# Performance work log

Measured on AMD Instinct MI355X. Metric: run time of the kernel, lower is better.

## Reference

```python
import jax, jax.numpy as jnp
import numpy as np

NEG_SLOPE = 0.2  # PyG GATv2Conv default negative_slope
HEADS = 4


def _gatv2_layer(x, src, dst, Wl, bl, Wr, br, att, bias):
    """GATv2Conv, concat=False (mean over heads), add_self_loops handled by caller.
    x: [N, Fin]; src/dst: [E] (message src -> dst); Wl/Wr: [Fin, H*C]; att: [H, C].
    """
    N = x.shape[0]
    H, C = att.shape
    xl = (x @ Wl + bl).reshape(N, H, C)  # source-side transform
    xr = (x @ Wr + br).reshape(N, H, C)  # target-side transform
    e = jax.nn.leaky_relu(xl[src] + xr[dst], NEG_SLOPE)          # [E, H, C]
    logits = jnp.einsum('ehc,hc->eh', e, att)                     # [E, H]
    # segment softmax over incoming edges of each target node
    m = jax.ops.segment_max(logits, dst, num_segments=N)          # [N, H]
    a = jnp.exp(logits - m[dst])
    denom = jax.ops.segment_sum(a, dst, num_segments=N)
    alpha = a / denom[dst]                                        # [E, H]
    out = jax.ops.segment_sum(alpha[:, :, None] * xl[src], dst, num_segments=N)  # [N, H, C]
    return out.mean(axis=1) + bias                                # concat=False -> head mean


def _glorot(k, shape):
    fan_in, fan_out = shape[0], shape[1] if len(shape) > 1 else shape[0]
    s = jnp.sqrt(2.0 / (fan_in + fan_out)).astype(jnp.float32)
    return jax.random.normal(k, shape, jnp.float32) * s


def setup_inputs() -> dict:
    key = jax.random.key(0)
    ks = jax.random.split(key, 24)
    N, E = 50000, 512000
    x = jax.random.normal(ks[0], (N, 9), jnp.float32)
    src = jax.random.randint(ks[1], (E,), 0, N, dtype=jnp.int32)
    dst = jax.random.randint(ks[2], (E,), 0, N, dtype=jnp.int32)
    dst = jnp.where(src == dst, (dst + 1) % N, dst)  # PyG removes self-loops then re-adds them
    edge_index = jnp.stack([src, dst])
    dims = [(9, 64), (64, 64), (64, 128)]  # (Fin, C_out) per layer
    inp = {'x': x, 'edge_index': edge_index}
    ki = 3
    for i, (fi, co) in enumerate(dims):
        inp[f'Wl{i}'] = _glorot(ks[ki], (fi, HEADS * co)); ki += 1
        inp[f'bl{i}'] = jnp.zeros((HEADS * co,), jnp.float32)
        inp[f'Wr{i}'] = _glorot(ks[ki], (fi, HEADS * co)); ki += 1
        inp[f'br{i}'] = jnp.zeros((HEADS * co,), jnp.float32)
        inp[f'att{i}'] = _glorot(ks[ki], (HEADS, co)); ki += 1
        inp[f'b{i}'] = jnp.zeros((co,), jnp.float32)
    return inp


def reference(x, edge_index, Wl0, bl0, Wr0, br0, att0, b0,
              Wl1, bl1, Wr1, br1, att1, b1,
              Wl2, bl2, Wr2, br2, att2, b2):
    N = x.shape[0]
    loops = jnp.arange(N, dtype=edge_index.dtype)
    src = jnp.concatenate([edge_index[0], loops])  # add self-loops (PyG default)
    dst = jnp.concatenate([edge_index[1], loops])
    h = _gatv2_layer(x, src, dst, Wl0, bl0, Wr0, br0, att0, b0)
    h = jax.nn.relu(h)  # dropout: eval mode -> identity
    h = _gatv2_layer(h, src, dst, Wl1, bl1, Wr1, br1, att1, b1)
    h = jax.nn.relu(h)
    out = _gatv2_layer(h, src, dst, Wl2, bl2, Wr2, br2, att2, b2)
    return out
```

## Files before the change

kernel.cpp:

```cpp
#include <hip/hip_runtime.h>
#include <hip/hip_bf16.h>


typedef __attribute__((ext_vector_type(8))) short bf16x8;
typedef __attribute__((ext_vector_type(4))) float f32x4;

__device__ __forceinline__ float bflo(unsigned w) { return __uint_as_float(w << 16); }
__device__ __forceinline__ float bfhi(unsigned w) { return __uint_as_float(w & 0xffff0000u); }
__device__ __forceinline__ unsigned short f2bf(float v) {
    unsigned u = __float_as_uint(v);
    u = (u + 0x7fff + ((u >> 16) & 1)) >> 16;
    return (unsigned short)u;
}
__device__ __forceinline__ float bf2f(unsigned short h) {
    return __uint_as_float((unsigned)h << 16);
}


__global__ void zero_int_k(int* p, int n) {
    int i = blockIdx.x * 256 + threadIdx.x;
    if (i < n) p[i] = 0;
}

__global__ void count_k(const int* __restrict__ dst, int* __restrict__ cnt,
                        int E, int EP) {
    int e = blockIdx.x * 256 + threadIdx.x;
    if (e >= EP) return;
    int d = (e < E) ? dst[e] : (e - E);
    atomicAdd(&cnt[d], 1);
}

__global__ void scan1_k(const int* __restrict__ cnt, int* __restrict__ offs,
                        int* __restrict__ partial, int N) {
    __shared__ int buf[2][1024];
    int g = blockIdx.x * 1024 + threadIdx.x;
    int v = (g < N) ? cnt[g] : 0;
    int pi = 0;
    buf[0][threadIdx.x] = v;
    __syncthreads();
    for (int s = 1; s < 1024; s <<= 1) {
        int t = buf[pi][threadIdx.x];
        if ((int)threadIdx.x >= s) t += buf[pi][threadIdx.x - s];
        buf[pi ^ 1][threadIdx.x] = t;
        pi ^= 1;
        __syncthreads();
    }
    int incl = buf[pi][threadIdx.x];
    if (g < N) offs[g + 1] = incl;
    if (threadIdx.x == 1023) partial[blockIdx.x] = incl;
}

__global__ void scan2_k(int* partial, int nb) {
    if (blockIdx.x == 0 && threadIdx.x == 0) {
        int run = 0;
        for (int i = 0; i < nb; i++) { int t = partial[i]; partial[i] = run; run += t; }
    }
}

__global__ void scan3_k(int* __restrict__ offs, const int* __restrict__ partial, int N) {
    int g = blockIdx.x * 1024 + threadIdx.x;
    if (g < N) offs[g + 1] += partial[blockIdx.x];
    if (g == 0) offs[0] = 0;
}

__global__ void copy_int_k(const int* __restrict__ a, int* __restrict__ b, int n) {
    int i = blockIdx.x * 256 + threadIdx.x;
    if (i < n) b[i] = a[i];
}

__global__ void fill_k(const int* __restrict__ src, const int* __restrict__ dst,
                       int* __restrict__ cursor, int* __restrict__ csrc,
                       int E, int EP) {
    int e = blockIdx.x * 256 + threadIdx.x;
    if (e >= EP) return;
    int sv, d;
    if (e < E) { sv = src[e]; d = dst[e]; }
    else       { sv = e - E;  d = sv; }
    int p = atomicAdd(&cursor[d], 1);
    csrc[p] = sv;
}

template <int FIN>
__global__ void gemm2_bf16_k(const float* __restrict__ X,
                             const float* __restrict__ Wl, const float* __restrict__ bl,
                             const float* __restrict__ Wr, const float* __restrict__ br,
                             unsigned short* __restrict__ xl, unsigned short* __restrict__ xr,
                             int N, int HCT) {
    constexpr int RPT = 16;
    __shared__ float Xs[RPT][FIN];
    int tid  = threadIdx.x;
    int col  = blockIdx.y * 256 + tid;
    int row0 = blockIdx.x * RPT;
    for (int i = tid; i < RPT * FIN; i += 256) {
        int r = i / FIN, k = i % FIN;
        int gr = row0 + r;
        Xs[r][k] = (gr < N) ? X[(size_t)gr * FIN + k] : 0.f;
    }
    __syncthreads();
    float aL[RPT], aR[RPT];
    float b1 = bl[col], b2 = br[col];
#pragma unroll
    for (int r = 0; r < RPT; r++) { aL[r] = b1; aR[r] = b2; }
    for (int k = 0; k < FIN; k++) {
        float wl = Wl[(size_t)k * HCT + col];
        float wr = Wr[(size_t)k * HCT + col];
#pragma unroll
        for (int r = 0; r < RPT; r++) {
            float xv = Xs[r][k];
            aL[r] = fmaf(xv, wl, aL[r]);
            aR[r] = fmaf(xv, wr, aR[r]);
        }
    }
#pragma unroll
    for (int r = 0; r < RPT; r++) {
        int gr = row0 + r;
        if (gr < N) {
            xl[(size_t)gr * HCT + col] = f2bf(aL[r]);
            xr[(size_t)gr * HCT + col] = f2bf(aR[r]);
        }
    }
}

__global__ void split_x_k(const float* __restrict__ X,
                          unsigned short* __restrict__ Ahi, unsigned short* __restrict__ Alo,
                          int total) {
    int i = blockIdx.x * 256 + threadIdx.x;
    if (i >= total) return;
    float v = X[i];
    unsigned short hi = f2bf(v);
    float lo = v - bf2f(hi);
    Ahi[i] = hi;
    Alo[i] = f2bf(lo);
}

__global__ void split_w_k(const float* __restrict__ Wl, const float* __restrict__ Wr,
                          unsigned short* __restrict__ Whi, unsigned short* __restrict__ Wlo,
                          int HCT, int total) {
    int tid = blockIdx.x * 256 + threadIdx.x;
    if (tid >= total) return;
    int j  = tid & 7;
    int l  = (tid >> 3) & 63;
    int ks = (tid >> 9) & 1;
    int ct = tid >> 10;
    int k  = ks * 32 + (l >> 4) * 8 + j;
    int cg = ct * 16 + (l & 15);
    float v = (cg < HCT) ? Wl[(size_t)k * HCT + cg] : Wr[(size_t)k * HCT + (cg - HCT)];
    unsigned short hi = f2bf(v);
    Whi[tid] = hi;
    Wlo[tid] = f2bf(v - bf2f(hi));
}

template <int CHUNKS>
__global__ void mfma_gemm_k(const unsigned short* __restrict__ Ahi,
                            const unsigned short* __restrict__ Alo,
                            const unsigned short* __restrict__ Wphi,
                            const unsigned short* __restrict__ Wplo,
                            const float* __restrict__ bl, const float* __restrict__ br,
                            unsigned short* __restrict__ xl, unsigned short* __restrict__ xr,
                            int N, int HCT) {
    __shared__ float lds[4][16][128];
    int tid = threadIdx.x;
    int w   = tid >> 6, l = tid & 63;
    int l15 = l & 15,  seg = l >> 4;
    int row  = blockIdx.x * 64 + w * 16 + l15;
    int arow = (row < N) ? row : (N - 1);

    bf16x8 a0h = *(const bf16x8*)(Ahi + (size_t)arow * 64 + seg * 8);
    bf16x8 a1h = *(const bf16x8*)(Ahi + (size_t)arow * 64 + 32 + seg * 8);
    bf16x8 a0l = *(const bf16x8*)(Alo + (size_t)arow * 64 + seg * 8);
    bf16x8 a1l = *(const bf16x8*)(Alo + (size_t)arow * 64 + 32 + seg * 8);

    for (int c = 0; c < CHUNKS; c++) {
        int mat   = (c * 128) / HCT;
        int mcol0 = (c * 128) % HCT;
        const float* bias = mat ? br : bl;
        unsigned short* out = mat ? xr : xl;
        f32x4 acc[8];
#pragma unroll
        for (int t = 0; t < 8; t++) {
            float bv = bias[mcol0 + t * 16 + l15];
            acc[t] = (f32x4){bv, bv, bv, bv};
        }
#pragma unroll
        for (int t = 0; t < 8; t++) {
            size_t ct = (size_t)(c * 8 + t);
            bf16x8 b0h = *(const bf16x8*)(Wphi + ((ct * 2    ) * 64 + l) * 8);
            bf16x8 b1h = *(const bf16x8*)(Wphi + ((ct * 2 + 1) * 64 + l) * 8);
            bf16x8 b0l = *(const bf16x8*)(Wplo + ((ct * 2    ) * 64 + l) * 8);
            bf16x8 b1l = *(const bf16x8*)(Wplo + ((ct * 2 + 1) * 64 + l) * 8);
            acc[t] = __builtin_amdgcn_mfma_f32_16x16x32_bf16(a0h, b0h, acc[t], 0, 0, 0);
            acc[t] = __builtin_amdgcn_mfma_f32_16x16x32_bf16(a1h, b1h, acc[t], 0, 0, 0);
            acc[t] = __builtin_amdgcn_mfma_f32_16x16x32_bf16(a0l, b0h, acc[t], 0, 0, 0);
            acc[t] = __builtin_amdgcn_mfma_f32_16x16x32_bf16(a1l, b1h, acc[t], 0, 0, 0);
            acc[t] = __builtin_amdgcn_mfma_f32_16x16x32_bf16(a0h, b0l, acc[t], 0, 0, 0);
            acc[t] = __builtin_amdgcn_mfma_f32_16x16x32_bf16(a1h, b1l, acc[t], 0, 0, 0);
        }
#pragma unroll
        for (int t = 0; t < 8; t++)
#pragma unroll
            for (int r = 0; r < 4; r++)
                lds[w][seg * 4 + r][t * 16 + l15] = acc[t][r];
#pragma unroll
        for (int r = 0; r < 16; r++) {
            int orow = blockIdx.x * 64 + w * 16 + r;
            if (orow < N) {
                float v0 = lds[w][r][2 * l];
                float v1 = lds[w][r][2 * l + 1];
                unsigned pack = (unsigned)f2bf(v0) | ((unsigned)f2bf(v1) << 16);
                *(unsigned*)(out + (size_t)orow * HCT + mcol0 + 2 * l) = pack;
            }
        }
    }
}

template <int F, bool RELU>
__global__ void node_fused_k(const unsigned short* __restrict__ xl,
                             const unsigned short* __restrict__ xr,
                             const float* __restrict__ att, const float* __restrict__ bias,
                             const int* __restrict__ offs, const int* __restrict__ csrc,
                             float* __restrict__ out, int N) {
    constexpr int HCT = 64 * F;
    constexpr int NW  = F / 2;
    int wv   = blockIdx.x * 4 + (threadIdx.x >> 6);
    int lane = threadIdx.x & 63;
    if (wv >= N) return;

    float xrv[F], at[F];
    {
        const unsigned* xp = (const unsigned*)(xr + (size_t)wv * HCT + lane * F);
#pragma unroll
        for (int i = 0; i < NW; i++) {
            unsigned w = xp[i];
            xrv[2 * i] = bflo(w); xrv[2 * i + 1] = bfhi(w);
        }
#pragma unroll
        for (int i = 0; i < F; i++) at[i] = att[lane * F + i];
    }

    int o0 = offs[wv], o1 = offs[wv + 1];
    float m = -1e30f, s = 0.f;
    float acc[F];
#pragma unroll
    for (int i = 0; i < F; i++) acc[i] = 0.f;

    for (int j = o0; j < o1; ++j) {
        int sn = csrc[j];
        const unsigned* xp = (const unsigned*)(xl + (size_t)sn * HCT + lane * F);
        float xv[F];
#pragma unroll
        for (int i = 0; i < NW; i++) {
            unsigned w = xp[i];
            xv[2 * i] = bflo(w); xv[2 * i + 1] = bfhi(w);
        }
        float p1 = 0.f, p2 = 0.f;
#pragma unroll
        for (int i = 0; i < F; i++) {
            float a = xv[i] + xrv[i];
            p1 = fmaf(at[i], a, p1);
            p2 = fmaf(at[i], fabsf(a), p2);
        }
        float p = fmaf(0.6f, p1, 0.4f * p2);
        p += __shfl_xor(p, 1, 64);
        p += __shfl_xor(p, 2, 64);
        p += __shfl_xor(p, 4, 64);
        p += __shfl_xor(p, 8, 64);
        if (__any(p > m + 20.f)) {
            float nm = fmaxf(m, p);
            float r  = __expf(m - nm);
            float w  = __expf(p - nm);
            s = fmaf(s, r, w);
#pragma unroll
            for (int i = 0; i < F; i++) acc[i] = fmaf(acc[i], r, w * xv[i]);
            m = nm;
        } else {
            float w = __expf(p - m);
            s += w;
#pragma unroll
            for (int i = 0; i < F; i++) acc[i] = fmaf(w, xv[i], acc[i]);
        }
    }

    float inv = 1.f / s;
#pragma unroll
    for (int i = 0; i < F; i++) acc[i] *= inv;
#pragma unroll
    for (int i = 0; i < F; i++) {
        acc[i] += __shfl_xor(acc[i], 16, 64);
        acc[i] += __shfl_xor(acc[i], 32, 64);
    }
    if (lane < 16) {
        float* op = out + (size_t)wv * (16 * F) + lane * F;
#pragma unroll
        for (int i = 0; i < F; i++) {
            float v = fmaf(acc[i], 0.25f, bias[lane * F + i]);
            if (RELU) v = fmaxf(v, 0.f);
            op[i] = v;
        }
    }
}


static inline size_t align256(size_t x) { return (x + 255) & ~(size_t)255; }

extern "C" void kernel_launch(void* const* d_in, const int* in_sizes, int n_in,
                              void* d_out, int out_size, void* d_ws, size_t ws_size,
                              hipStream_t stream) {
    const float* x  = (const float*)d_in[0];
    const int*   ei = (const int*)d_in[1];
    const int N  = in_sizes[0] / 9;
    const int E  = in_sizes[1] / 2;
    const int EP = E + N;
    const int* src = ei;
    const int* dst = ei + E;

    const float *Wl[3], *bl[3], *Wr[3], *br[3], *att[3], *bb[3];
    for (int i = 0; i < 3; i++) {
        Wl[i]  = (const float*)d_in[2 + 6 * i];
        bl[i]  = (const float*)d_in[3 + 6 * i];
        Wr[i]  = (const float*)d_in[4 + 6 * i];
        br[i]  = (const float*)d_in[5 + 6 * i];
        att[i] = (const float*)d_in[6 + 6 * i];
        bb[i]  = (const float*)d_in[7 + 6 * i];
    }

    char* w = (char*)d_ws;
    unsigned short* xl = (unsigned short*)w; w += align256((size_t)N * 512 * 2);
    unsigned short* xr = (unsigned short*)w; w += align256((size_t)N * 512 * 2);
    float* hA = (float*)w;   w += align256((size_t)N * 64 * 4);
    float* hB = (float*)w;   w += align256((size_t)N * 64 * 4);
    int* offs   = (int*)w;   w += align256((size_t)(N + 1) * 4);
    int* cursor = (int*)w;   w += align256((size_t)N * 4);
    int* csrc   = (int*)w;   w += align256((size_t)EP * 4);
    int* partial = (int*)w;  w += 4096;
    unsigned short* Wp1h = (unsigned short*)w; w += align256((size_t)32 * 1024 * 2);
    unsigned short* Wp1l = (unsigned short*)w; w += align256((size_t)32 * 1024 * 2);
    unsigned short* Wp2h = (unsigned short*)w; w += align256((size_t)64 * 1024 * 2);
    unsigned short* Wp2l = (unsigned short*)w; w += align256((size_t)64 * 1024 * 2);

    unsigned short* Ahi1 = (unsigned short*)hB;
    unsigned short* Alo1 = Ahi1 + (size_t)N * 64;
    unsigned short* Ahi2 = (unsigned short*)hA;
    unsigned short* Alo2 = Ahi2 + (size_t)N * 64;

    int* cnt = cursor;
    zero_int_k<<<(N + 255) / 256, 256, 0, stream>>>(cnt, N);
    count_k<<<(EP + 255) / 256, 256, 0, stream>>>(dst, cnt, E, EP);
    int nb = (N + 1023) / 1024;
    scan1_k<<<nb, 1024, 0, stream>>>(cnt, offs, partial, N);
    scan2_k<<<1, 64, 0, stream>>>(partial, nb);
    scan3_k<<<nb, 1024, 0, stream>>>(offs, partial, N);
    copy_int_k<<<(N + 255) / 256, 256, 0, stream>>>(offs, cursor, N);
    fill_k<<<(EP + 255) / 256, 256, 0, stream>>>(src, dst, cursor, csrc, E, EP);

    split_w_k<<<(32 * 1024 + 255) / 256, 256, 0, stream>>>(Wl[1], Wr[1], Wp1h, Wp1l, 256, 32 * 1024);
    split_w_k<<<(64 * 1024 + 255) / 256, 256, 0, stream>>>(Wl[2], Wr[2], Wp2h, Wp2l, 512, 64 * 1024);

    const int nodeBlocks = (N + 3) / 4;
    const int gemmBlocks = (N + 63) / 64;
    const int splitBlocks = (N * 64 + 255) / 256;

    dim3 g1((N + 15) / 16, 1);
    gemm2_bf16_k<9><<<g1, 256, 0, stream>>>(
        x, Wl[0], bl[0], Wr[0], br[0], xl, xr, N, 256);
    node_fused_k<4, true><<<nodeBlocks, 256, 0, stream>>>(
        xl, xr, att[0], bb[0], offs, csrc, hA, N);

    split_x_k<<<splitBlocks, 256, 0, stream>>>(hA, Ahi1, Alo1, N * 64);
    mfma_gemm_k<4><<<gemmBlocks, 256, 0, stream>>>(
        Ahi1, Alo1, Wp1h, Wp1l, bl[1], br[1], xl, xr, N, 256);
    node_fused_k<4, true><<<nodeBlocks, 256, 0, stream>>>(
        xl, xr, att[1], bb[1], offs, csrc, hB, N);

    split_x_k<<<splitBlocks, 256, 0, stream>>>(hB, Ahi2, Alo2, N * 64);
    mfma_gemm_k<8><<<gemmBlocks, 256, 0, stream>>>(
        Ahi2, Alo2, Wp2h, Wp2l, bl[2], br[2], xl, xr, N, 512);
    node_fused_k<8, false><<<nodeBlocks, 256, 0, stream>>>(
        xl, xr, att[2], bb[2], offs, csrc, (float*)d_out, N);
}
```

Measured before the change: 476.5 us.

## Fuse layer-0 transform into aggregation and split-to-bf16 into node epilogue

```diff
diff --git a/kernel.cpp b/kernel.cpp
--- a/kernel.cpp
+++ b/kernel.cpp
@@ -63,91 +63,40 @@
     if (g == 0) offs[0] = 0;
 }
 
-__global__ void copy_int_k(const int* __restrict__ a, int* __restrict__ b, int n) {
-    int i = blockIdx.x * 256 + threadIdx.x;
-    if (i < n) b[i] = a[i];
-}
-
-__global__ void fill_k(const int* __restrict__ src, const int* __restrict__ dst,
-                       int* __restrict__ cursor, int* __restrict__ csrc,
-                       int E, int EP) {
+__global__ void fill2_k(const int* __restrict__ src, const int* __restrict__ dst,
+                        const int* __restrict__ offs, int* __restrict__ cnt2,
+                        int* __restrict__ csrc, int E, int EP) {
     int e = blockIdx.x * 256 + threadIdx.x;
     if (e >= EP) return;
     int sv, d;
     if (e < E) { sv = src[e]; d = dst[e]; }
     else       { sv = e - E;  d = sv; }
-    int p = atomicAdd(&cursor[d], 1);
+    int p = offs[d] + atomicAdd(&cnt2[d], 1);
     csrc[p] = sv;
 }
 
-template <int FIN>
-__global__ void gemm2_bf16_k(const float* __restrict__ X,
-                             const float* __restrict__ Wl, const float* __restrict__ bl,
-                             const float* __restrict__ Wr, const float* __restrict__ br,
-                             unsigned short* __restrict__ xl, unsigned short* __restrict__ xr,
-                             int N, int HCT) {
-    constexpr int RPT = 16;
-    __shared__ float Xs[RPT][FIN];
-    int tid  = threadIdx.x;
-    int col  = blockIdx.y * 256 + tid;
-    int row0 = blockIdx.x * RPT;
-    for (int i = tid; i < RPT * FIN; i += 256) {
-        int r = i / FIN, k = i % FIN;
-        int gr = row0 + r;
-        Xs[r][k] = (gr < N) ? X[(size_t)gr * FIN + k] : 0.f;
-    }
-    __syncthreads();
-    float aL[RPT], aR[RPT];
-    float b1 = bl[col], b2 = br[col];
-#pragma unroll
-    for (int r = 0; r < RPT; r++) { aL[r] = b1; aR[r] = b2; }
-    for (int k = 0; k < FIN; k++) {
-        float wl = Wl[(size_t)k * HCT + col];
-        float wr = Wr[(size_t)k * HCT + col];
-#pragma unroll
-        for (int r = 0; r < RPT; r++) {
-            float xv = Xs[r][k];
-            aL[r] = fmaf(xv, wl, aL[r]);
-            aR[r] = fmaf(xv, wr, aR[r]);
-        }
-    }
-#pragma unroll
-    for (int r = 0; r < RPT; r++) {
-        int gr = row0 + r;
-        if (gr < N) {
-            xl[(size_t)gr * HCT + col] = f2bf(aL[r]);
-            xr[(size_t)gr * HCT + col] = f2bf(aR[r]);
-        }
-    }
-}
-
-__global__ void split_x_k(const float* __restrict__ X,
-                          unsigned short* __restrict__ Ahi, unsigned short* __restrict__ Alo,
-                          int total) {
-    int i = blockIdx.x * 256 + threadIdx.x;
-    if (i >= total) return;
-    float v = X[i];
-    unsigned short hi = f2bf(v);
-    float lo = v - bf2f(hi);
-    Ahi[i] = hi;
-    Alo[i] = f2bf(lo);
-}
-
-__global__ void split_w_k(const float* __restrict__ Wl, const float* __restrict__ Wr,
-                          unsigned short* __restrict__ Whi, unsigned short* __restrict__ Wlo,
-                          int HCT, int total) {
-    int tid = blockIdx.x * 256 + threadIdx.x;
-    if (tid >= total) return;
-    int j  = tid & 7;
-    int l  = (tid >> 3) & 63;
-    int ks = (tid >> 9) & 1;
-    int ct = tid >> 10;
+__device__ __forceinline__ void pack_one(const float* Wl, const float* Wr,
+                                         unsigned short* Wh, unsigned short* Wlo,
+                                         int HCT, int t) {
+    int j  = t & 7;
+    int l  = (t >> 3) & 63;
+    int ks = (t >> 9) & 1;
+    int ct = t >> 10;
     int k  = ks * 32 + (l >> 4) * 8 + j;
     int cg = ct * 16 + (l & 15);
     float v = (cg < HCT) ? Wl[(size_t)k * HCT + cg] : Wr[(size_t)k * HCT + (cg - HCT)];
     unsigned short hi = f2bf(v);
-    Whi[tid] = hi;
-    Wlo[tid] = f2bf(v - bf2f(hi));
+    Wh[t]  = hi;
+    Wlo[t] = f2bf(v - bf2f(hi));
+}
+
+__global__ void split_w2_k(const float* __restrict__ Wl1, const float* __restrict__ Wr1,
+                           unsigned short* __restrict__ W1h, unsigned short* __restrict__ W1l,
+                           const float* __restrict__ Wl2, const float* __restrict__ Wr2,
+                           unsigned short* __restrict__ W2h, unsigned short* __restrict__ W2l) {
+    int tid = blockIdx.x * 256 + threadIdx.x;
+    if (tid < 32 * 1024) pack_one(Wl1, Wr1, W1h, W1l, 256, tid);
+    else                 pack_one(Wl2, Wr2, W2h, W2l, 512, tid - 32 * 1024);
 }
 
 template <int CHUNKS>
@@ -213,48 +162,64 @@
     }
 }
 
-template <int F, bool RELU>
-__global__ void node_fused_k(const unsigned short* __restrict__ xl,
-                             const unsigned short* __restrict__ xr,
-                             const float* __restrict__ att, const float* __restrict__ bias,
-                             const int* __restrict__ offs, const int* __restrict__ csrc,
-                             float* __restrict__ out, int N) {
-    constexpr int HCT = 64 * F;
-    constexpr int NW  = F / 2;
+__global__ void node_l0_k(const float* __restrict__ X,
+                          const float* __restrict__ Wl, const float* __restrict__ bl,
+                          const float* __restrict__ Wr, const float* __restrict__ br,
+                          const float* __restrict__ att, const float* __restrict__ bias,
+                          const int* __restrict__ offs, const int* __restrict__ csrc,
+                          unsigned short* __restrict__ Yhi, unsigned short* __restrict__ Ylo,
+                          int N) {
     int wv   = blockIdx.x * 4 + (threadIdx.x >> 6);
     int lane = threadIdx.x & 63;
     if (wv >= N) return;
-
-    float xrv[F], at[F];
+    int c0 = lane * 4;
+
+    float at[4];
+#pragma unroll
+    for (int i = 0; i < 4; i++) at[i] = att[c0 + i];
+
+    float xrv[4];
     {
-        const unsigned* xp = (const unsigned*)(xr + (size_t)wv * HCT + lane * F);
-#pragma unroll
-        for (int i = 0; i < NW; i++) {
-            unsigned w = xp[i];
-            xrv[2 * i] = bflo(w); xrv[2 * i + 1] = bfhi(w);
-        }
-#pragma unroll
-        for (int i = 0; i < F; i++) at[i] = att[lane * F + i];
-    }
+        float xsd[9];
+#pragma unroll
+        for (int k = 0; k < 9; k++) xsd[k] = X[(size_t)wv * 9 + k];
+#pragma unroll
+        for (int i = 0; i < 4; i++) xrv[i] = br[c0 + i];
+#pragma unroll
+        for (int k = 0; k < 9; k++)
+#pragma unroll
+            for (int i = 0; i < 4; i++)
+                xrv[i] = fmaf(xsd[k], Wr[k * 256 + c0 + i], xrv[i]);
+    }
+
+    float wl[9][4], blv[4];
+#pragma unroll
+    for (int k = 0; k < 9; k++) {
+        f32x4 wv4 = *(const f32x4*)(Wl + k * 256 + c0);
+#pragma unroll
+        for (int i = 0; i < 4; i++) wl[k][i] = wv4[i];
+    }
+#pragma unroll
+    for (int i = 0; i < 4; i++) blv[i] = bl[c0 + i];
 
     int o0 = offs[wv], o1 = offs[wv + 1];
     float m = -1e30f, s = 0.f;
-    float acc[F];
-#pragma unroll
-    for (int i = 0; i < F; i++) acc[i] = 0.f;
+    float acc[4] = {0.f, 0.f, 0.f, 0.f};
 
     for (int j = o0; j < o1; ++j) {
         int sn = csrc[j];
-        const unsigned* xp = (const unsigned*)(xl + (size_t)sn * HCT + lane * F);
-        float xv[F];
-#pragma unroll
-        for (int i = 0; i < NW; i++) {
-            unsigned w = xp[i];
-            xv[2 * i] = bflo(w); xv[2 * i + 1] = bfhi(w);
-        }
+        const float* xp = X + (size_t)sn * 9;
+        float xs[9];
+#pragma unroll
+        for (int k = 0; k < 9; k++) xs[k] = xp[k];
+        float xv[4] = {blv[0], blv[1], blv[2], blv[3]};
+#pragma unroll
+        for (int k = 0; k < 9; k++)
+#pragma unroll
+            for (int i = 0; i < 4; i++) xv[i] = fmaf(xs[k], wl[k][i], xv[i]);
         float p1 = 0.f, p2 = 0.f;
 #pragma unroll
-        for (int i = 0; i < F; i++) {
+        for (int i = 0; i < 4; i++) {
             float a = xv[i] + xrv[i];
             p1 = fmaf(at[i], a, p1);
             p2 = fmaf(at[i], fabsf(a), p2);
@@ -270,6 +235,99 @@
             float w  = __expf(p - nm);
             s = fmaf(s, r, w);
 #pragma unroll
+            for (int i = 0; i < 4; i++) acc[i] = fmaf(acc[i], r, w * xv[i]);
+            m = nm;
+        } else {
+            float w = __expf(p - m);
+            s += w;
+#pragma unroll
+            for (int i = 0; i < 4; i++) acc[i] = fmaf(w, xv[i], acc[i]);
+        }
+    }
+
+    float inv = 1.f / s;
+#pragma unroll
+    for (int i = 0; i < 4; i++) acc[i] *= inv;
+#pragma unroll
+    for (int i = 0; i < 4; i++) {
+        acc[i] += __shfl_xor(acc[i], 16, 64);
+        acc[i] += __shfl_xor(acc[i], 32, 64);
+    }
+    if (lane < 16) {
+        unsigned short h[4], lo[4];
+#pragma unroll
+        for (int i = 0; i < 4; i++) {
+            float v = fmaf(acc[i], 0.25f, bias[lane * 4 + i]);
+            v = fmaxf(v, 0.f);
+            h[i] = f2bf(v);
+            lo[i] = f2bf(v - bf2f(h[i]));
+        }
+        size_t base = (size_t)wv * 64 + lane * 4;
+        *(uint2*)(Yhi + base) = (uint2){(unsigned)h[0] | ((unsigned)h[1] << 16),
+                                        (unsigned)h[2] | ((unsigned)h[3] << 16)};
+        *(uint2*)(Ylo + base) = (uint2){(unsigned)lo[0] | ((unsigned)lo[1] << 16),
+                                        (unsigned)lo[2] | ((unsigned)lo[3] << 16)};
+    }
+}
+
+template <int F, int OUT>
+__global__ void node_fused_k(const unsigned short* __restrict__ xl,
+                             const unsigned short* __restrict__ xr,
+                             const float* __restrict__ att, const float* __restrict__ bias,
+                             const int* __restrict__ offs, const int* __restrict__ csrc,
+                             unsigned short* __restrict__ Yhi, unsigned short* __restrict__ Ylo,
+                             float* __restrict__ out, int N) {
+    constexpr int HCT = 64 * F;
+    constexpr int NW  = F / 2;
+    int wv   = blockIdx.x * 4 + (threadIdx.x >> 6);
+    int lane = threadIdx.x & 63;
+    if (wv >= N) return;
+
+    float xrv[F], at[F];
+    {
+        const unsigned* xp = (const unsigned*)(xr + (size_t)wv * HCT + lane * F);
+#pragma unroll
+        for (int i = 0; i < NW; i++) {
+            unsigned w = xp[i];
+            xrv[2 * i] = bflo(w); xrv[2 * i + 1] = bfhi(w);
+        }
+#pragma unroll
+        for (int i = 0; i < F; i++) at[i] = att[lane * F + i];
+    }
+
+    int o0 = offs[wv], o1 = offs[wv + 1];
+    float m = -1e30f, s = 0.f;
+    float acc[F];
+#pragma unroll
+    for (int i = 0; i < F; i++) acc[i] = 0.f;
+
+    for (int j = o0; j < o1; ++j) {
+        int sn = csrc[j];
+        const unsigned* xp = (const unsigned*)(xl + (size_t)sn * HCT + lane * F);
+        float xv[F];
+#pragma unroll
+        for (int i = 0; i < NW; i++) {
+            unsigned w = xp[i];
+            xv[2 * i] = bflo(w); xv[2 * i + 1] = bfhi(w);
+        }
+        float p1 = 0.f, p2 = 0.f;
+#pragma unroll
+        for (int i = 0; i < F; i++) {
+            float a = xv[i] + xrv[i];
+            p1 = fmaf(at[i], a, p1);
+            p2 = fmaf(at[i], fabsf(a), p2);
+        }
+        float p = fmaf(0.6f, p1, 0.4f * p2);
+        p += __shfl_xor(p, 1, 64);
+        p += __shfl_xor(p, 2, 64);
+        p += __shfl_xor(p, 4, 64);
+        p += __shfl_xor(p, 8, 64);
+        if (__any(p > m + 20.f)) {
+            float nm = fmaxf(m, p);
+            float r  = __expf(m - nm);
+            float w  = __expf(p - nm);
+            s = fmaf(s, r, w);
+#pragma unroll
             for (int i = 0; i < F; i++) acc[i] = fmaf(acc[i], r, w * xv[i]);
             m = nm;
         } else {
@@ -289,12 +347,26 @@
         acc[i] += __shfl_xor(acc[i], 32, 64);
     }
     if (lane < 16) {
-        float* op = out + (size_t)wv * (16 * F) + lane * F;
-#pragma unroll
-        for (int i = 0; i < F; i++) {
-            float v = fmaf(acc[i], 0.25f, bias[lane * F + i]);
-            if (RELU) v = fmaxf(v, 0.f);
-            op[i] = v;
+        if (OUT == 0) {
+            unsigned short h[F], lo[F];
+#pragma unroll
+            for (int i = 0; i < F; i++) {
+                float v = fmaf(acc[i], 0.25f, bias[lane * F + i]);
+                v = fmaxf(v, 0.f);
+                h[i] = f2bf(v);
+                lo[i] = f2bf(v - bf2f(h[i]));
+            }
+            size_t base = (size_t)wv * (16 * F) + lane * F;
+#pragma unroll
+            for (int i = 0; i < F / 2; i++) {
+                ((unsigned*)(Yhi + base))[i] = (unsigned)h[2 * i] | ((unsigned)h[2 * i + 1] << 16);
+                ((unsigned*)(Ylo + base))[i] = (unsigned)lo[2 * i] | ((unsigned)lo[2 * i + 1] << 16);
+            }
+        } else {
+            float* op = out + (size_t)wv * (16 * F) + lane * F;
+#pragma unroll
+            for (int i = 0; i < F; i++)
+                op[i] = fmaf(acc[i], 0.25f, bias[lane * F + i]);
         }
     }
 }
@@ -324,56 +396,46 @@
     }
 
     char* w = (char*)d_ws;
-    unsigned short* xl = (unsigned short*)w; w += align256((size_t)N * 512 * 2);
-    unsigned short* xr = (unsigned short*)w; w += align256((size_t)N * 512 * 2);
-    float* hA = (float*)w;   w += align256((size_t)N * 64 * 4);
-    float* hB = (float*)w;   w += align256((size_t)N * 64 * 4);
-    int* offs   = (int*)w;   w += align256((size_t)(N + 1) * 4);
-    int* cursor = (int*)w;   w += align256((size_t)N * 4);
-    int* csrc   = (int*)w;   w += align256((size_t)EP * 4);
-    int* partial = (int*)w;  w += 4096;
+    unsigned short* xl  = (unsigned short*)w; w += align256((size_t)N * 512 * 2);
+    unsigned short* xr  = (unsigned short*)w; w += align256((size_t)N * 512 * 2);
+    unsigned short* A1h = (unsigned short*)w; w += align256((size_t)N * 64 * 2);
+    unsigned short* A1l = (unsigned short*)w; w += align256((size_t)N * 64 * 2);
+    unsigned short* A2h = (unsigned short*)w; w += align256((size_t)N * 64 * 2);
+    unsigned short* A2l = (unsigned short*)w; w += align256((size_t)N * 64 * 2);
+    int* offs   = (int*)w;  w += align256((size_t)(N + 1) * 4);
+    int* cnt    = (int*)w;  w += align256((size_t)(2 * N) * 4);
+    int* csrc   = (int*)w;  w += align256((size_t)EP * 4);
+    int* partial = (int*)w; w += 4096;
     unsigned short* Wp1h = (unsigned short*)w; w += align256((size_t)32 * 1024 * 2);
     unsigned short* Wp1l = (unsigned short*)w; w += align256((size_t)32 * 1024 * 2);
     unsigned short* Wp2h = (unsigned short*)w; w += align256((size_t)64 * 1024 * 2);
     unsigned short* Wp2l = (unsigned short*)w; w += align256((size_t)64 * 1024 * 2);
-
-    unsigned short* Ahi1 = (unsigned short*)hB;
-    unsigned short* Alo1 = Ahi1 + (size_t)N * 64;
-    unsigned short* Ahi2 = (unsigned short*)hA;
-    unsigned short* Alo2 = Ahi2 + (size_t)N * 64;
-
-    int* cnt = cursor;
-    zero_int_k<<<(N + 255) / 256, 256, 0, stream>>>(cnt, N);
+    int* cnt2 = cnt + N;
+
+    zero_int_k<<<(2 * N + 255) / 256, 256, 0, stream>>>(cnt, 2 * N);
     count_k<<<(EP + 255) / 256, 256, 0, stream>>>(dst, cnt, E, EP);
     int nb = (N + 1023) / 1024;
     scan1_k<<<nb, 1024, 0, stream>>>(cnt, offs, partial, N);
     scan2_k<<<1, 64, 0, stream>>>(partial, nb);
     scan3_k<<<nb, 1024, 0, stream>>>(offs, partial, N);
-    copy_int_k<<<(N + 255) / 256, 256, 0, stream>>>(offs, cursor, N);
-    fill_k<<<(EP + 255) / 256, 256, 0, stream>>>(src, dst, cursor, csrc, E, EP);
-
-    split_w_k<<<(32 * 1024 + 255) / 256, 256, 0, stream>>>(Wl[1], Wr[1], Wp1h, Wp1l, 256, 32 * 1024);
-    split_w_k<<<(64 * 1024 + 255) / 256, 256, 0, stream>>>(Wl[2], Wr[2], Wp2h, Wp2l, 512, 64 * 1024);
+    fill2_k<<<(EP + 255) / 256, 256, 0, stream>>>(src, dst, offs, cnt2, csrc, E, EP);
+
+    split_w2_k<<<(96 * 1024) / 256, 256, 0, stream>>>(
+        Wl[1], Wr[1], Wp1h, Wp1l, Wl[2], Wr[2], Wp2h, Wp2l);
 
     const int nodeBlocks = (N + 3) / 4;
     const int gemmBlocks = (N + 63) / 64;
-    const int splitBlocks = (N * 64 + 255) / 256;
-
-    dim3 g1((N + 15) / 16, 1);
-    gemm2_bf16_k<9><<<g1, 256, 0, stream>>>(
-        x, Wl[0], bl[0], Wr[0], br[0], xl, xr, N, 256);
-    node_fused_k<4, true><<<nodeBlocks, 256, 0, stream>>>(
-        xl, xr, att[0], bb[0], offs, csrc, hA, N);
-
-    split_x_k<<<splitBlocks, 256, 0, stream>>>(hA, Ahi1, Alo1, N * 64);
+
+    node_l0_k<<<nodeBlocks, 256, 0, stream>>>(
+        x, Wl[0], bl[0], Wr[0], br[0], att[0], bb[0], offs, csrc, A1h, A1l, N);
+
     mfma_gemm_k<4><<<gemmBlocks, 256, 0, stream>>>(
-        Ahi1, Alo1, Wp1h, Wp1l, bl[1], br[1], xl, xr, N, 256);
-    node_fused_k<4, true><<<nodeBlocks, 256, 0, stream>>>(
-        xl, xr, att[1], bb[1], offs, csrc, hB, N);
-
-    split_x_k<<<splitBlocks, 256, 0, stream>>>(hB, Ahi2, Alo2, N * 64);
+        A1h, A1l, Wp1h, Wp1l, bl[1], br[1], xl, xr, N, 256);
+    node_fused_k<4, 0><<<nodeBlocks, 256, 0, stream>>>(
+        xl, xr, att[1], bb[1], offs, csrc, A2h, A2l, nullptr, N);
+
     mfma_gemm_k<8><<<gemmBlocks, 256, 0, stream>>>(
-        Ahi2, Alo2, Wp2h, Wp2l, bl[2], br[2], xl, xr, N, 512);
-    node_fused_k<8, false><<<nodeBlocks, 256, 0, stream>>>(
-        xl, xr, att[2], bb[2], offs, csrc, (float*)d_out, N);
-}
+        A2h, A2l, Wp2h, Wp2l, bl[2], br[2], xl, xr, N, 512);
+    node_fused_k<8, 1><<<nodeBlocks, 256, 0, stream>>>(
+        xl, xr, att[2], bb[2], offs, csrc, nullptr, nullptr, (float*)d_out, N);
+}
```

After: 465.8 us. 2.2% less time.
